# Kernel optimization log

Hardware: AMD Instinct MI355X
Metric: run time of the kernel (lower is better)

The kernel has to match this reference:

```python
import jax, jax.numpy as jnp
import numpy as np

DN = ('NCHW', 'OIHW', 'NCHW')

def _conv(x, w, stride, pad, groups=1):
    return jax.lax.conv_general_dilated(x, w, (stride, stride), pad,
                                        feature_group_count=groups,
                                        dimension_numbers=DN)

def _bn(x, s, b):
    # eval-mode BatchNorm folded to per-channel affine
    return x * s[:, None, None] + b[:, None, None]

def _gelu(x):
    return jax.nn.gelu(x, approximate=False)  # torch nn.GELU default = exact erf

def _region_dw(x, dw_w, s1, b1, pw_w, s2, b2, g):
    # Vectorized RegionLayerDW: split [B,C,H,W] into g*g tiles, apply per-tile
    # depthwise3x3 -> BN -> GELU -> 1x1 -> BN -> +residual, reassemble.
    B, C, H, W = x.shape
    th, tw = H // g, W // g
    t = x.reshape(B, C, g, th, g, tw).transpose(2, 4, 0, 1, 3, 5)
    t = t.reshape(g * g, B, C, th, tw)  # [G,B,C,th,tw]
    def tile(xt, w, ts1, tb1, pw, ts2, tb2):
        h = _conv(xt, w, 1, ((1, 1), (1, 1)), groups=C)  # depthwise 3x3
        h = _gelu(_bn(h, ts1, tb1))
        h = jnp.einsum('bchw,oc->bohw', h, pw)  # 1x1 conv
        return _bn(h, ts2, tb2) + xt
    y = jax.vmap(tile)(t, dw_w, s1, b1, pw_w, s2, b2)
    y = y.reshape(g, g, B, C, th, tw).transpose(2, 3, 0, 4, 1, 5)
    return y.reshape(B, C, H, W)

def _forward(x, r1_w, r1_s, r1_b, r1_dw, r1_s1, r1_b1, r1_pw, r1_s2, r1_b2,
             r2_w, r2_s, r2_b, r2_dw, r2_s1, r2_b1, r2_pw, r2_s2, r2_b2,
             h1_w1, h1_s1, h1_b1, h1_w2, h1_s2, h1_b2, h1_w3, h1_s3, h1_b3,
             h2_w1, h2_s1, h2_b1, h2_w2, h2_s2, h2_b2,
             h3_w, h3_s, h3_b):
    B = x.shape[0]
    # region1: 5x5 conv 3->24, BN, GELU, RegionLayerDW grid 7x7; then outer GELU
    r1 = _gelu(_bn(_conv(x, r1_w, 1, ((2, 2), (2, 2))), r1_s, r1_b))
    r1 = _region_dw(r1, r1_dw, r1_s1, r1_b1, r1_pw, r1_s2, r1_b2, 7)
    region1 = _gelu(r1)
    # region2: 3x3 conv 24->48, BN, GELU, RegionLayerDW grid 4x4; outer GELU
    r2 = _gelu(_bn(_conv(region1, r2_w, 1, ((1, 1), (1, 1))), r2_s, r2_b))
    r2 = _region_dw(r2, r2_dw, r2_s1, r2_b1, r2_pw, r2_s2, r2_b2, 4)
    region2 = _gelu(r2)
    # hMLP branch1: 3 -> 48(k4s4) -> 48(k2s2) -> 256(k2s2)
    h = _gelu(_bn(_conv(x, h1_w1, 4, 'VALID'), h1_s1, h1_b1))
    h = _gelu(_bn(_conv(h, h1_w2, 2, 'VALID'), h1_s2, h1_b2))
    branch1 = _bn(_conv(h, h1_w3, 2, 'VALID'), h1_s3, h1_b3)
    # hMLP branch2: 24 -> 48(k4s4) -> 256(k4s4)
    g2 = _gelu(_bn(_conv(region1, h2_w1, 4, 'VALID'), h2_s1, h2_b1))
    branch2 = _bn(_conv(g2, h2_w2, 4, 'VALID'), h2_s2, h2_b2)
    # hMLP branch3: 48 -> 256(k16s16)
    branch3 = _bn(_conv(region2, h3_w, 16, 'VALID'), h3_s, h3_b)
    out = jnp.concatenate((branch1, branch2, branch3), axis=1)  # [B,768,14,14]
    return jnp.transpose(out.reshape(B, out.shape[1], -1), (0, 2, 1))  # [B,196,768]


def setup_inputs() -> dict:
    key = jax.random.key(0)
    ks = [key]
    def nk():
        ks[0], k = jax.random.split(ks[0])
        return k
    def rn(shape, scale=0.05):
        return jax.random.normal(nk(), shape, jnp.float32) * scale
    def sc(shape):
        return 1.0 + rn(shape)
    B = 16
    d = {}
    d['x'] = rn((B, 3, 224, 224), 1.0)
    d['r1_w'] = rn((24, 3, 5, 5)); d['r1_s'] = sc((24,)); d['r1_b'] = rn((24,))
    d['r1_dw'] = rn((49, 24, 1, 3, 3)); d['r1_s1'] = sc((49, 24)); d['r1_b1'] = rn((49, 24))
    d['r1_pw'] = rn((49, 24, 24)); d['r1_s2'] = sc((49, 24)); d['r1_b2'] = rn((49, 24))
    d['r2_w'] = rn((48, 24, 3, 3)); d['r2_s'] = sc((48,)); d['r2_b'] = rn((48,))
    d['r2_dw'] = rn((16, 48, 1, 3, 3)); d['r2_s1'] = sc((16, 48)); d['r2_b1'] = rn((16, 48))
    d['r2_pw'] = rn((16, 48, 48)); d['r2_s2'] = sc((16, 48)); d['r2_b2'] = rn((16, 48))
    d['h1_w1'] = rn((48, 3, 4, 4)); d['h1_s1'] = sc((48,)); d['h1_b1'] = rn((48,))
    d['h1_w2'] = rn((48, 48, 2, 2)); d['h1_s2'] = sc((48,)); d['h1_b2'] = rn((48,))
    d['h1_w3'] = rn((256, 48, 2, 2)); d['h1_s3'] = sc((256,)); d['h1_b3'] = rn((256,))
    d['h2_w1'] = rn((48, 24, 4, 4)); d['h2_s1'] = sc((48,)); d['h2_b1'] = rn((48,))
    d['h2_w2'] = rn((256, 48, 4, 4)); d['h2_s2'] = sc((256,)); d['h2_b2'] = rn((256,))
    d['h3_w'] = rn((256, 48, 16, 16)); d['h3_s'] = sc((256,)); d['h3_b'] = rn((256,))
    return d


def reference(x, r1_w, r1_s, r1_b, r1_dw, r1_s1, r1_b1, r1_pw, r1_s2, r1_b2,
              r2_w, r2_s, r2_b, r2_dw, r2_s1, r2_b1, r2_pw, r2_s2, r2_b2,
              h1_w1, h1_s1, h1_b1, h1_w2, h1_s2, h1_b2, h1_w3, h1_s3, h1_b3,
              h2_w1, h2_s1, h2_b1, h2_w2, h2_s2, h2_b2,
              h3_w, h3_s, h3_b):
    return _forward(x, r1_w, r1_s, r1_b, r1_dw, r1_s1, r1_b1, r1_pw, r1_s2, r1_b2,
                    r2_w, r2_s, r2_b, r2_dw, r2_s1, r2_b1, r2_pw, r2_s2, r2_b2,
                    h1_w1, h1_s1, h1_b1, h1_w2, h1_s2, h1_b2, h1_w3, h1_s3, h1_b3,
                    h2_w1, h2_s1, h2_b1, h2_w2, h2_s2, h2_b2,
                    h3_w, h3_s, h3_b)
```

## Files before the change

kernel.cpp:

```cpp
#include <hip/hip_runtime.h>
#include <hip/hip_bf16.h>
#include <math.h>

typedef __attribute__((ext_vector_type(8))) short short8;
typedef __attribute__((ext_vector_type(4))) float f32x4;

__device__ __forceinline__ float gelu_f(float x) {
  float s = x * x;
  float w = __builtin_fmaf(s, 0.10294196f, 2.30220795f);
  float e = __builtin_amdgcn_exp2f(x * w);
  float r = __builtin_amdgcn_rcpf(1.0f + e);
  return __builtin_fmaf(-x, r, x);
}

template<bool TBL, bool GELU, bool TOOUT>
__global__ __launch_bounds__(256) void convgemm_k(
    const float* __restrict__ in, const float* __restrict__ w,
    const float* __restrict__ bns, const float* __restrict__ bnb,
    float* __restrict__ out,
    int Cin, int H, int W, int ks, int stride, int pad, int ls,
    int OH, int OW, int N, int K, int ch0) {
  __shared__ __align__(16) float sA[16][64];
  __shared__ __align__(16) float sB[16][64];
  __shared__ int sTbl[256];
  const int tid = threadIdx.x;
  if (TBL) {
    int kk2 = ks * ks;
    for (int k = tid; k < K; k += 256) {
      int ic = k / kk2, r = k - ic * kk2;
      sTbl[k] = (ic << 16) | ((r / ks) << 8) | (r % ks);
    }
  }
  const int m0 = blockIdx.x * 64, n0 = blockIdx.y * 64;
  const int mm = tid >> 2, kq = tid & 3;
  const int OHW = OH * OW, HW = H * W;
  int m = m0 + mm;
  int bI = m / OHW; int r = m - bI * OHW;
  int oh = r / OW;  int ow = r - oh * OW;
  const int ihBase = oh * stride - pad, iwBase = ow * stride - pad;
  const int inBase = bI * Cin * HW;
  const int tm = tid & 15, tn = tid >> 4;
  float acc[4][4] = {};
  for (int k0 = 0; k0 < K; k0 += 16) {
    __syncthreads();
#pragma unroll
    for (int i = 0; i < 4; ++i) {
      int kk = kq * 4 + i, k = k0 + kk;
      float v = 0.0f;
      if (k < K) {
        int ic, dy, dx;
        if (TBL) {
          int tv = sTbl[k]; ic = tv >> 16; dy = (tv >> 8) & 255; dx = tv & 255;
        } else {
          ic = k >> (2 * ls);
          int r2 = k & ((1 << (2 * ls)) - 1);
          dy = r2 >> ls; dx = r2 & ((1 << ls) - 1);
        }
        int ih = ihBase + dy, iw = iwBase + dx;
        if (ih >= 0 && ih < H && iw >= 0 && iw < W)
          v = in[inBase + ic * HW + ih * W + iw];
      }
      sA[kk][mm] = v;
    }
#pragma unroll
    for (int i = 0; i < 4; ++i) {
      int kk = kq * 4 + i, k = k0 + kk;
      int n = n0 + mm;
      float v = 0.0f;
      if (n < N && k < K) v = w[n * K + k];
      sB[kk][mm] = v;
    }
    __syncthreads();
#pragma unroll
    for (int kk = 0; kk < 16; ++kk) {
      float4 a4 = *(const float4*)&sA[kk][tm * 4];
      float4 b4 = *(const float4*)&sB[kk][tn * 4];
      acc[0][0] += a4.x * b4.x; acc[0][1] += a4.x * b4.y;
      acc[0][2] += a4.x * b4.z; acc[0][3] += a4.x * b4.w;
      acc[1][0] += a4.y * b4.x; acc[1][1] += a4.y * b4.y;
      acc[1][2] += a4.y * b4.z; acc[1][3] += a4.y * b4.w;
      acc[2][0] += a4.z * b4.x; acc[2][1] += a4.z * b4.y;
      acc[2][2] += a4.z * b4.z; acc[2][3] += a4.z * b4.w;
      acc[3][0] += a4.w * b4.x; acc[3][1] += a4.w * b4.y;
      acc[3][2] += a4.w * b4.z; acc[3][3] += a4.w * b4.w;
    }
  }
#pragma unroll
  for (int i = 0; i < 4; ++i) {
    int mI = m0 + tm * 4 + i;
    int bO = mI / OHW; int rr = mI - bO * OHW;
#pragma unroll
    for (int j = 0; j < 4; ++j) {
      int n = n0 + tn * 4 + j;
      if (n < N) {
        float v = acc[i][j] * bns[n] + bnb[n];
        if (GELU) v = gelu_f(v);
        if (TOOUT) {
          out[(bO * OHW + rr) * 768 + ch0 + n] = v;
        } else {
          int oh2 = rr / OW, ow2 = rr - oh2 * OW;
          out[((bO * N + n) * OH + oh2) * OW + ow2] = v;
        }
      }
    }
  }
}

template<int CIN, int KS, int STRIDE, int PAD, int NN, int KP, bool GELU,
         int OUTMODE, int NVALID = NN>
__global__ __launch_bounds__(256) void nhwc_conv_mfma(
    const __hip_bfloat16* __restrict__ in, const __hip_bfloat16* __restrict__ wb,
    const float* __restrict__ bns, const float* __restrict__ bnb,
    float* __restrict__ out, int Hin, int Win, int OW, int OHW) {
  constexpr int K = KS * KS * CIN;
  constexpr int LROW = KP + 8;
  __shared__ __align__(16) __hip_bfloat16 sA[64][LROW];
  __shared__ __align__(16) __hip_bfloat16 sB[NN][LROW];
  const int tid = threadIdx.x;
  const float4 f4z = make_float4(0.f, 0.f, 0.f, 0.f);
  if constexpr (CIN == 4) {
    const int m = tid & 63, tg = tid >> 6;
    const int mg = blockIdx.x * 64 + m;
    const int bI = mg / OHW; int pix = mg - bI * OHW;
    const int oh = pix / OW, ow = pix - oh * OW;
    for (int dy = tg; dy < KS; dy += 4) {
      const int ih = oh * STRIDE - PAD + dy;
      __hip_bfloat16* dst = &sA[m][dy * KS * 4];
#pragma unroll
      for (int j = 0; j < KS; ++j) {
        int iw = ow * STRIDE - PAD + j;
        uint2 v = make_uint2(0u, 0u);
        if (ih >= 0 && ih < Hin && iw >= 0 && iw < Win)
          v = *(const uint2*)(in + (((size_t)bI * Hin + ih) * Win + iw) * 4);
        *(uint2*)(dst + j * 4) = v;
      }
    }
    if (tg == 3) {
      for (int c = K; c < KP; c += 4) *(uint2*)&sA[m][c] = make_uint2(0u, 0u);
    }
  } else {
    const int m = tid & 63, dy = tid >> 6;
    const int mg = blockIdx.x * 64 + m;
    const int bI = mg / OHW; int pix = mg - bI * OHW;
    const int oh = pix / OW, ow = pix - oh * OW;
    if (dy < KS) {
      const int ih = oh * STRIDE - PAD + dy;
      __hip_bfloat16* dst = &sA[m][dy * KS * CIN];
      if (ih < 0 || ih >= Hin) {
#pragma unroll
        for (int i = 0; i < KS * CIN / 8; ++i) ((float4*)dst)[i] = f4z;
      } else {
        const __hip_bfloat16* srow = in + ((size_t)bI * Hin + ih) * Win * CIN;
#pragma unroll
        for (int j = 0; j < KS; ++j) {
          int iw = ow * STRIDE - PAD + j;
          if (PAD > 0 && (iw < 0 || iw >= Win)) {
#pragma unroll
            for (int i = 0; i < CIN / 8; ++i) ((float4*)(dst + j * CIN))[i] = f4z;
          } else {
            const float4* s4 = (const float4*)(srow + (size_t)iw * CIN);
#pragma unroll
            for (int i = 0; i < CIN / 8; ++i) ((float4*)(dst + j * CIN))[i] = s4[i];
          }
        }
      }
    } else if (K < KP) {
#pragma unroll
      for (int c = K; c < KP + 8; c += 8) *(float4*)&sA[m][c] = f4z;
    }
  }
  {
    constexpr int NV = NN * KP / 8;
    const float4* w4 = (const float4*)wb;
    for (int i = tid; i < NV; i += 256) {
      int n = i / (KP / 8), c = i - n * (KP / 8);
      *(float4*)&sB[n][c * 8] = w4[i];
    }
  }
  __syncthreads();
  constexpr int NT = NN / 16;
  const int wave = tid >> 6, lane = tid & 63;
  const int fm = lane & 15, quad = lane >> 4;
  const int wm = wave * 16;
  f32x4 acc[NT] = {};
#pragma unroll
  for (int ks = 0; ks < KP / 32; ++ks) {
    short8 a = *(const short8*)&sA[wm + fm][ks * 32 + quad * 8];
#pragma unroll
    for (int j = 0; j < NT; ++j) {
      short8 b = *(const short8*)&sB[j * 16 + fm][ks * 32 + quad * 8];
      acc[j] = __builtin_amdgcn_mfma_f32_16x16x32_bf16(a, b, acc[j], 0, 0, 0);
    }
  }
  const int mg0 = blockIdx.x * 64 + wm + quad * 4;
  const int bI = mg0 / OHW, pix = mg0 - bI * OHW;
#pragma unroll
  for (int j = 0; j < NT; ++j) {
    int n = j * 16 + fm;
    if (n >= NVALID) continue;
    float s = bns[n], bb = bnb[n];
    float v[4];
#pragma unroll
    for (int e = 0; e < 4; ++e) {
      v[e] = acc[j][e] * s + bb;
      if (GELU) v[e] = gelu_f(v[e]);
    }
    if (OUTMODE == 0) {
      float4 v4 = make_float4(v[0], v[1], v[2], v[3]);
      *(float4*)&out[((size_t)(bI * NVALID + n)) * OHW + pix] = v4;
    } else {
      __hip_bfloat16* ob = (__hip_bfloat16*)out;
#pragma unroll
      for (int e = 0; e < 4; ++e)
        ob[((size_t)(bI * OHW + pix + e)) * NVALID + n] = (__hip_bfloat16)v[e];
    }
  }
}

__global__ __launch_bounds__(256, 4) void conv5_tile_mfma(
    const __hip_bfloat16* __restrict__ in,
    const __hip_bfloat16* __restrict__ wb,
    const float* __restrict__ bns, const float* __restrict__ bnb,
    __hip_bfloat16* __restrict__ out) {
  __shared__ __align__(16) __hip_bfloat16 sHalo[13][144];
  __shared__ __align__(16) __hip_bfloat16 sW5[32][128];
  __shared__ float sS[24], sBb[24];
  const int tid = threadIdx.x;
  const int X0 = blockIdx.x * 32, Y0 = blockIdx.y * 8, b = blockIdx.z;
  {
    const float4* w4 = (const float4*)wb;
    for (int i = tid; i < 512; i += 256) {
      int n = i >> 4, g = i & 15;
      *(float4*)&sW5[n][(g ^ (n & 7)) * 8] = w4[i];
    }
  }
  if (tid < 24) { sS[tid] = bns[tid]; sBb[tid] = bnb[tid]; }
  for (int i = tid; i < 468; i += 256) {
    int r = i / 36, p = i - r * 36;
    int iy = Y0 - 2 + r, ix = X0 - 2 + p;
    uint2 v = make_uint2(0u, 0u);
    if (r < 12 && iy >= 0 && iy < 224 && ix >= 0 && ix < 224)
      v = *(const uint2*)(in + (((size_t)b * 224 + iy) * 224 + ix) * 4);
    *(uint2*)&sHalo[r][p * 4] = v;
  }
  __syncthreads();
  const int wave = tid >> 6, lane = tid & 63;
  const int fm = lane & 15, quad = lane >> 4;
  f32x4 acc[4][2] = {};
#pragma unroll
  for (int ks = 0; ks < 4; ++ks) {
    const int k0 = ks * 32 + quad * 8;
    const int dy = k0 / 24, u = k0 - dy * 24;
    const int grp = ks * 4 + quad;
    short8 wfr[2];
#pragma unroll
    for (int cg = 0; cg < 2; ++cg) {
      int wr = cg * 16 + fm;
      wfr[cg] = *(const short8*)&sW5[wr][(grp ^ (wr & 7)) * 8];
    }
#pragma unroll
    for (int pg = 0; pg < 4; ++pg) {
      const int r = 2 * wave + (pg >> 1);
      const int c = (pg & 1) * 16 + fm;
      short8 pf = *(const short8*)&sHalo[r + dy][c * 4 + u];
#pragma unroll
      for (int cg = 0; cg < 2; ++cg)
        acc[pg][cg] = __builtin_amdgcn_mfma_f32_16x16x32_bf16(
            wfr[cg], pf, acc[pg][cg], 0, 0, 0);
    }
  }
#pragma unroll
  for (int pg = 0; pg < 4; ++pg) {
    const int row = Y0 + 2 * wave + (pg >> 1);
    const int col = X0 + (pg & 1) * 16 + fm;
    __hip_bfloat16* obase = out + (((size_t)b * 224 + row) * 224 + col) * 24;
#pragma unroll
    for (int cg = 0; cg < 2; ++cg) {
      const int ch0 = cg * 16 + quad * 4;
      if (ch0 < 24) {
        __hip_bfloat16 vb[4];
#pragma unroll
        for (int e = 0; e < 4; ++e) {
          float v = acc[pg][cg][e] * sS[ch0 + e] + sBb[ch0 + e];
          vb[e] = (__hip_bfloat16)gelu_f(v);
        }
        *(uint2*)&obase[ch0] = *(uint2*)vb;
      }
    }
  }
}

__global__ __launch_bounds__(256, 4) void conv3_tile_mfma(
    const __hip_bfloat16* __restrict__ in,
    const __hip_bfloat16* __restrict__ wb,
    const float* __restrict__ bns, const float* __restrict__ bnb,
    __hip_bfloat16* __restrict__ out) {
  __shared__ __align__(16) __hip_bfloat16 sIn[11][816];
  __shared__ __align__(16) __hip_bfloat16 sB[48][232];
  __shared__ float sS[48], sBb[48];
  const int tid = threadIdx.x;
  const int X0 = blockIdx.x * 32, Y0 = blockIdx.y * 8, b = blockIdx.z;
  {
    const float4* w4 = (const float4*)wb;
    for (int i = tid; i < 1344; i += 256) {
      int n = i / 28, c = i - n * 28;
      *(float4*)&sB[n][c * 8] = w4[i];
    }
  }
  if (tid < 48) { sS[tid] = bns[tid]; sBb[tid] = bnb[tid]; }
  for (int i = tid; i < 1020; i += 256) {
    int r = i / 102, c8 = i - r * 102;
    int p = c8 / 3;
    int iy = Y0 - 1 + r, ix = X0 - 1 + p;
    uint4 v = make_uint4(0u, 0u, 0u, 0u);
    if (iy >= 0 && iy < 224 && ix >= 0 && ix < 224)
      v = *(const uint4*)(in + (((size_t)b * 224 + iy) * 224 + ix) * 24 +
                          (c8 - p * 3) * 8);
    *(uint4*)&sIn[r][c8 * 8] = v;
  }
  for (int i = tid; i < 102; i += 256)
    *(uint4*)&sIn[10][i * 8] = make_uint4(0u, 0u, 0u, 0u);
  __syncthreads();
  const int wave = tid >> 6, lane = tid & 63;
  const int fm = lane & 15, quad = lane >> 4;
  f32x4 acc[4][3] = {};
#pragma unroll
  for (int ks = 0; ks < 7; ++ks) {
    const int k0 = ks * 32 + quad * 8;
    const int dy = k0 / 72;
    const int u = k0 - dy * 72;
    short8 wfr[3];
#pragma unroll
    for (int cg = 0; cg < 3; ++cg)
      wfr[cg] = *(const short8*)&sB[cg * 16 + fm][k0];
#pragma unroll
    for (int pg = 0; pg < 4; ++pg) {
      const int r = 2 * wave + (pg >> 1);
      const int c = (pg & 1) * 16 + fm;
      short8 pf = *(const short8*)&sIn[r + dy][c * 24 + u];
#pragma unroll
      for (int cg = 0; cg < 3; ++cg)
        acc[pg][cg] = __builtin_amdgcn_mfma_f32_16x16x32_bf16(
            wfr[cg], pf, acc[pg][cg], 0, 0, 0);
    }
  }
#pragma unroll
  for (int pg = 0; pg < 4; ++pg) {
    const int row = Y0 + 2 * wave + (pg >> 1);
    const int col = X0 + (pg & 1) * 16 + fm;
    __hip_bfloat16* obase = out + (((size_t)b * 224 + row) * 224 + col) * 48;
#pragma unroll
    for (int cg = 0; cg < 3; ++cg) {
      const int ch0 = cg * 16 + quad * 4;
      __hip_bfloat16 vb[4];
#pragma unroll
      for (int e = 0; e < 4; ++e) {
        const int ch = ch0 + e;
        float v = acc[pg][cg][e] * sS[ch] + sBb[ch];
        vb[e] = (__hip_bfloat16)gelu_f(v);
      }
      *(uint2*)&obase[ch0] = *(uint2*)vb;
    }
  }
}

__global__ __launch_bounds__(256, 4) void region2_mfma(
    const __hip_bfloat16* __restrict__ in, const float* __restrict__ dww,
    const float* __restrict__ s1v, const float* __restrict__ b1v,
    const __hip_bfloat16* __restrict__ pwb,
    const float* __restrict__ s2v, const float* __restrict__ b2v,
    __hip_bfloat16* __restrict__ out) {
  __shared__ __align__(16) __hip_bfloat16 sIn[10][10][56];
  __shared__ __align__(16) __hip_bfloat16 sH[64][64];
  __shared__ __align__(16) __hip_bfloat16 sW[48][64];
  __shared__ float sDW[48][9];
  __shared__ float sS1[48], sB1[48], sS2[48], sB2[48];
  const int t = blockIdx.x, sb = blockIdx.y, b = blockIdx.z;
  const int gy = t >> 2, gx = t & 3;
  const int py0 = (sb / 7) * 8, px0 = (sb % 7) * 8;
  const int Y0 = gy * 56, X0 = gx * 56;
  const int tid = threadIdx.x;
  for (int i = tid; i < 48 * 8; i += 256) {
    int n = i >> 3, g = i & 7;
    float4 v = *(const float4*)&pwb[(size_t)(t * 48 + n) * 64 + g * 8];
    *(float4*)&sW[n][((g ^ (n & 7)) * 8)] = v;
  }
  for (int i = tid; i < 432; i += 256) ((float*)sDW)[i] = dww[t * 432 + i];
  if (tid < 48) {
    sS1[tid] = s1v[t * 48 + tid]; sB1[tid] = b1v[t * 48 + tid];
    sS2[tid] = s2v[t * 48 + tid]; sB2[tid] = b2v[t * 48 + tid];
  }
  for (int i = tid; i < 600; i += 256) {
    int px = i / 6, grp = i - px * 6;
    int r = px / 10, c = px - r * 10;
    int ly = py0 + r - 1, lx = px0 + c - 1;
    uint4 v = make_uint4(0u, 0u, 0u, 0u);
    if (ly >= 0 && ly < 56 && lx >= 0 && lx < 56)
      v = *(const uint4*)(in + (((size_t)b * 224 + Y0 + ly) * 224 + X0 + lx) * 48 +
                          grp * 8);
    *(uint4*)&sIn[r][c][grp * 8] = v;
  }
  __syncthreads();
  if (tid < 192) {
    const int cg = tid >> 4;
    const int rem = tid & 15;
    const int col = rem >> 1;
    const int rh = rem & 1;
    const int ch0 = cg * 4;
    float wv[4][9], s14[4], b14[4];
#pragma unroll
    for (int c4 = 0; c4 < 4; ++c4) {
#pragma unroll
      for (int q = 0; q < 9; ++q) wv[c4][q] = sDW[ch0 + c4][q];
      s14[c4] = sS1[ch0 + c4]; b14[c4] = sB1[ch0 + c4];
    }
    float win[3][12];
#pragma unroll
    for (int rr = 0; rr < 6; ++rr) {
      int r = rh * 4 + rr;
      float* wr = win[rr % 3];
#pragma unroll
      for (int cc = 0; cc < 3; ++cc) {
        uint2 u = *(const uint2*)&sIn[r][col + cc][ch0];
        wr[cc * 4 + 0] = __uint_as_float(u.x << 16);
        wr[cc * 4 + 1] = __uint_as_float(u.x & 0xffff0000u);
        wr[cc * 4 + 2] = __uint_as_float(u.y << 16);
        wr[cc * 4 + 3] = __uint_as_float(u.y & 0xffff0000u);
      }
      if (rr >= 2) {
        const float* ra = win[(rr - 2) % 3];
        const float* rb = win[(rr - 1) % 3];
        const float* rc = win[rr % 3];
        int px = (rh * 4 + rr - 2) * 8 + col;
        __hip_bfloat16 hv[4];
#pragma unroll
        for (int c4 = 0; c4 < 4; ++c4) {
          float a = ra[c4] * wv[c4][0] + ra[4 + c4] * wv[c4][1] + ra[8 + c4] * wv[c4][2]
                  + rb[c4] * wv[c4][3] + rb[4 + c4] * wv[c4][4] + rb[8 + c4] * wv[c4][5]
                  + rc[c4] * wv[c4][6] + rc[4 + c4] * wv[c4][7] + rc[8 + c4] * wv[c4][8];
          hv[c4] = (__hip_bfloat16)gelu_f(a * s14[c4] + b14[c4]);
        }
        *(uint2*)&sH[px][((cg >> 1) ^ (px & 7)) * 8 + (cg & 1) * 4] = *(uint2*)hv;
      }
    }
  } else {
    for (int i = tid - 192; i < 128; i += 64) {
      int px = i >> 1, g = 6 + (i & 1);
      *(float4*)&sH[px][(g ^ (px & 7)) * 8] = make_float4(0.f, 0.f, 0.f, 0.f);
    }
  }
  __syncthreads();
  const int wave = tid >> 6, lane = tid & 63;
  const int fm = lane & 15, quad = lane >> 4;
  const int px = wave * 16 + fm, pxk = px & 7;
  f32x4 acc[3] = {};
#pragma unroll
  for (int ks = 0; ks < 2; ++ks) {
    short8 hb = *(const short8*)&sH[px][((ks * 4 + quad) ^ pxk) * 8];
#pragma unroll
    for (int m = 0; m < 3; ++m) {
      int wr = m * 16 + fm;
      short8 wa = *(const short8*)&sW[wr][((ks * 4 + quad) ^ (wr & 7)) * 8];
      acc[m] = __builtin_amdgcn_mfma_f32_16x16x32_bf16(wa, hb, acc[m], 0, 0, 0);
    }
  }
  const int row = px >> 3, col = px & 7;
  __hip_bfloat16* obase =
      out + (((size_t)b * 224 + Y0 + py0 + row) * 224 + X0 + px0 + col) * 48;
#pragma unroll
  for (int m = 0; m < 3; ++m) {
    int ch0m = m * 16 + quad * 4;
    uint2 ru = *(const uint2*)&sIn[row + 1][col + 1][ch0m];
    float res[4];
    res[0] = __uint_as_float(ru.x << 16);
    res[1] = __uint_as_float(ru.x & 0xffff0000u);
    res[2] = __uint_as_float(ru.y << 16);
    res[3] = __uint_as_float(ru.y & 0xffff0000u);
    __hip_bfloat16 vb[4];
#pragma unroll
    for (int e = 0; e < 4; ++e) {
      int ch = ch0m + e;
      float v = acc[m][e] * sS2[ch] + sB2[ch] + res[e];
      vb[e] = (__hip_bfloat16)gelu_f(v);
    }
    *(uint2*)&obase[ch0m] = *(uint2*)vb;
  }
}

__global__ __launch_bounds__(256, 4) void region1_mfma(
    const __hip_bfloat16* __restrict__ in, const float* __restrict__ dww,
    const float* __restrict__ s1v, const float* __restrict__ b1v,
    const __hip_bfloat16* __restrict__ pwb,
    const float* __restrict__ s2v, const float* __restrict__ b2v,
    __hip_bfloat16* __restrict__ out) {
  __shared__ __align__(16) __hip_bfloat16 sIn[10][10][24];
  __shared__ __align__(16) __hip_bfloat16 sH[64][32];
  __shared__ __align__(16) __hip_bfloat16 sW[32][32];
  __shared__ float sDW[24][9];
  __shared__ float sS1[24], sB1[24], sS2[24], sB2[24];
  const int t = blockIdx.x, sb = blockIdx.y, b = blockIdx.z;
  const int gy = t / 7, gx = t % 7;
  const int py0 = (sb >> 2) * 8, px0 = (sb & 3) * 8;
  const int Y0 = gy * 32, X0 = gx * 32;
  const int tid = threadIdx.x;
  for (int i = tid; i < 128; i += 256) {
    int n = i >> 2, g = i & 3;
    float4 v = make_float4(0.f, 0.f, 0.f, 0.f);
    if (n < 24) v = *(const float4*)&pwb[(size_t)(t * 24 + n) * 32 + g * 8];
    *(float4*)&sW[n][(g ^ (n & 3)) * 8] = v;
  }
  for (int i = tid; i < 216; i += 256) ((float*)sDW)[i] = dww[t * 216 + i];
  if (tid < 24) {
    sS1[tid] = s1v[t * 24 + tid]; sB1[tid] = b1v[t * 24 + tid];
    sS2[tid] = s2v[t * 24 + tid]; sB2[tid] = b2v[t * 24 + tid];
  }
  for (int i = tid; i < 300; i += 256) {
    int px = i / 3, grp = i - px * 3;
    int r = px / 10, c = px - r * 10;
    int ly = py0 + r - 1, lx = px0 + c - 1;
    uint4 v = make_uint4(0u, 0u, 0u, 0u);
    if (ly >= 0 && ly < 32 && lx >= 0 && lx < 32)
      v = *(const uint4*)(in + (((size_t)b * 224 + Y0 + ly) * 224 + X0 + lx) * 24 +
                          grp * 8);
    *(uint4*)&sIn[r][c][grp * 8] = v;
  }
  __syncthreads();
  if (tid < 192) {
    const int cg = tid >> 5;
    const int rem = tid & 31;
    const int col = rem >> 2;
    const int rq = rem & 3;
    const int ch0 = cg * 4;
    float wv[4][9], s14[4], b14[4];
#pragma unroll
    for (int c4 = 0; c4 < 4; ++c4) {
#pragma unroll
      for (int q = 0; q < 9; ++q) wv[c4][q] = sDW[ch0 + c4][q];
      s14[c4] = sS1[ch0 + c4]; b14[c4] = sB1[ch0 + c4];
    }
    float win[3][12];
#pragma unroll
    for (int rr = 0; rr < 4; ++rr) {
      int r = rq * 2 + rr;
      float* wr = win[rr % 3];
#pragma unroll
      for (int cc = 0; cc < 3; ++cc) {
        uint2 u = *(const uint2*)&sIn[r][col + cc][ch0];
        wr[cc * 4 + 0] = __uint_as_float(u.x << 16);
        wr[cc * 4 + 1] = __uint_as_float(u.x & 0xffff0000u);
        wr[cc * 4 + 2] = __uint_as_float(u.y << 16);
        wr[cc * 4 + 3] = __uint_as_float(u.y & 0xffff0000u);
      }
      if (rr >= 2) {
        const float* ra = win[(rr - 2) % 3];
        const float* rb = win[(rr - 1) % 3];
        const float* rc = win[rr % 3];
        int px = (rq * 2 + rr - 2) * 8 + col;
        __hip_bfloat16 hv[4];
#pragma unroll
        for (int c4 = 0; c4 < 4; ++c4) {
          float a = ra[c4] * wv[c4][0] + ra[4 + c4] * wv[c4][1] + ra[8 + c4] * wv[c4][2]
                  + rb[c4] * wv[c4][3] + rb[4 + c4] * wv[c4][4] + rb[8 + c4] * wv[c4][5]
                  + rc[c4] * wv[c4][6] + rc[4 + c4] * wv[c4][7] + rc[8 + c4] * wv[c4][8];
          hv[c4] = (__hip_bfloat16)gelu_f(a * s14[c4] + b14[c4]);
        }
        *(uint2*)&sH[px][((cg >> 1) ^ (px & 3)) * 8 + (cg & 1) * 4] = *(uint2*)hv;
      }
    }
  } else {
    int px = tid - 192;
    *(float4*)&sH[px][(3 ^ (px & 3)) * 8] = make_float4(0.f, 0.f, 0.f, 0.f);
  }
  __syncthreads();
  const int wave = tid >> 6, lane = tid & 63;
  const int fm = lane & 15, quad = lane >> 4;
  const int px = wave * 16 + fm;
  short8 hb = *(const short8*)&sH[px][(quad ^ (px & 3)) * 8];
  f32x4 acc[2] = {};
#pragma unroll
  for (int m = 0; m < 2; ++m) {
    int wr = m * 16 + fm;
    short8 wa = *(const short8*)&sW[wr][(quad ^ (wr & 3)) * 8];
    acc[m] = __builtin_amdgcn_mfma_f32_16x16x32_bf16(wa, hb, acc[m], 0, 0, 0);
  }
  const int row = px >> 3, col = px & 7;
  __hip_bfloat16* obase =
      out + (((size_t)b * 224 + Y0 + py0 + row) * 224 + X0 + px0 + col) * 24;
#pragma unroll
  for (int m = 0; m < 2; ++m) {
    int ch0m = m * 16 + quad * 4;
    if (ch0m < 24) {
      uint2 ru = *(const uint2*)&sIn[row + 1][col + 1][ch0m];
      float res[4];
      res[0] = __uint_as_float(ru.x << 16);
      res[1] = __uint_as_float(ru.x & 0xffff0000u);
      res[2] = __uint_as_float(ru.y << 16);
      res[3] = __uint_as_float(ru.y & 0xffff0000u);
      __hip_bfloat16 vb[4];
#pragma unroll
      for (int e = 0; e < 4; ++e) {
        int ch = ch0m + e;
        float v = acc[m][e] * sS2[ch] + sB2[ch] + res[e];
        vb[e] = (__hip_bfloat16)gelu_f(v);
      }
      *(uint2*)&obase[ch0m] = *(uint2*)vb;
    }
  }
}

template<int PS, int IMGW, int KTOT, int KSL, bool ATOMIC>
__global__ __launch_bounds__(256) void patch_gemm_mfma(
    const __hip_bfloat16* __restrict__ A, const __hip_bfloat16* __restrict__ Wb,
    const float* __restrict__ scale, const float* __restrict__ bias,
    float* __restrict__ out, int M, int ch0) {
  constexpr int RUN = PS * 48;
  __shared__ __align__(16) __hip_bfloat16 sA[64][64];
  __shared__ __align__(16) __hip_bfloat16 sB[64][64];
  const int tid = threadIdx.x;
  const int m0 = blockIdx.x * 64, n0 = blockIdx.y * 64;
  const int kBase = blockIdx.z * KSL;
  const int mi = tid >> 2, seg = tid & 3;
  int m = m0 + mi; int mc = (m < M) ? m : (M - 1);
  int bI = mc / 196; int r = mc - bI * 196;
  int oh = r / 14, ow = r - oh * 14;
  const __hip_bfloat16* Abase =
      A + (((size_t)bI * IMGW + oh * PS) * IMGW + ow * PS) * 48;
  const __hip_bfloat16* Wrow = Wb + (size_t)(n0 + mi) * KTOT;
  const int wave = tid >> 6, lane = tid & 63;
  const int wm = (wave & 1) * 32, wn = (wave >> 1) * 32;
  const int fm = lane & 15, quad = lane >> 4;
  const int sw = fm & 7;
  f32x4 acc[2][2] = {};
  for (int k0 = kBase; k0 < kBase + KSL; k0 += 64) {
    int dy = k0 / RUN, rem = k0 - dy * RUN;
    __syncthreads();
    {
      const __hip_bfloat16* p = Abase + (size_t)dy * IMGW * 48 + rem + seg * 16;
      float4 v0 = *(const float4*)p;
      float4 v1 = *(const float4*)(p + 8);
      int key = mi & 7;
      *(float4*)&sA[mi][((seg * 2) ^ key) * 8] = v0;
      *(float4*)&sA[mi][((seg * 2 + 1) ^ key) * 8] = v1;
      const __hip_bfloat16* q = Wrow + k0 + seg * 16;
      float4 w0 = *(const float4*)q;
      float4 w1 = *(const float4*)(q + 8);
      *(float4*)&sB[mi][((seg * 2) ^ key) * 8] = w0;
      *(float4*)&sB[mi][((seg * 2 + 1) ^ key) * 8] = w1;
    }
    __syncthreads();
#pragma unroll
    for (int ks = 0; ks < 2; ++ks) {
      int cg = (ks * 4 + quad) ^ sw;
#pragma unroll
      for (int i = 0; i < 2; ++i) {
        short8 a = *(const short8*)&sA[wm + i * 16 + fm][cg * 8];
#pragma unroll
        for (int j = 0; j < 2; ++j) {
          short8 b = *(const short8*)&sB[wn + j * 16 + fm][cg * 8];
          acc[i][j] = __builtin_amdgcn_mfma_f32_16x16x32_bf16(a, b, acc[i][j], 0, 0, 0);
        }
      }
    }
  }
#pragma unroll
  for (int i = 0; i < 2; ++i) {
#pragma unroll
    for (int j = 0; j < 2; ++j) {
      int gn = n0 + wn + j * 16 + fm;
      float sc = scale[gn];
#pragma unroll
      for (int e = 0; e < 4; ++e) {
        int gm = m0 + wm + i * 16 + quad * 4 + e;
        if (gm < M) {
          if (ATOMIC)
            atomicAdd(&out[(size_t)gm * 768 + ch0 + gn], acc[i][j][e] * sc);
          else
            out[(size_t)gm * 768 + ch0 + gn] = acc[i][j][e] * sc + bias[gn];
        }
      }
    }
  }
}

__device__ __forceinline__ void reorder_wk_el(
    const float* __restrict__ w, __hip_bfloat16* __restrict__ o,
    int i, int N, int Cin, int ks, int KP) {
  if (i >= N * KP) return;
  int n = i / KP, k = i - n * KP;
  float v = 0.f;
  int K = ks * ks * Cin;
  if (k < K) {
    int dy = k / (ks * Cin); int r = k - dy * ks * Cin;
    int dx = r / Cin, ic = r - dx * Cin;
    v = w[((n * Cin + ic) * ks + dy) * ks + dx];
  }
  o[i] = (__hip_bfloat16)v;
}

__global__ __launch_bounds__(256) void prep_all(
    const float* __restrict__ x, __hip_bfloat16* __restrict__ xb,
    const float* __restrict__ h3_w, __hip_bfloat16* __restrict__ h3wb,
    const float* __restrict__ r2_w, __hip_bfloat16* __restrict__ r2wb,
    const float* __restrict__ h2_w1, __hip_bfloat16* __restrict__ h2w1b,
    const float* __restrict__ h2_w2, __hip_bfloat16* __restrict__ h2w2b,
    const float* __restrict__ r1_w, __hip_bfloat16* __restrict__ r1wb,
    const float* __restrict__ r2_pw, __hip_bfloat16* __restrict__ pw2wb,
    const float* __restrict__ r1_pw, __hip_bfloat16* __restrict__ pw1wb,
    const float* __restrict__ h1_w1, __hip_bfloat16* __restrict__ h1w1b,
    const float* __restrict__ h3_b, float* __restrict__ out) {
  __shared__ __hip_bfloat16 sL[12288];
  const int blk = blockIdx.x, tid = threadIdx.x;
  if (blk < 3136) {
    int i = blk * 256 + tid;
    int b = i / 50176, p = i - b * 50176;
    const float* src = x + (size_t)b * 150528 + p;
    __hip_bfloat16 v[4];
    v[0] = (__hip_bfloat16)src[0];
    v[1] = (__hip_bfloat16)src[50176];
    v[2] = (__hip_bfloat16)src[100352];
    v[3] = (__hip_bfloat16)0.0f;
    *(uint2*)&xb[(size_t)i * 4] = *(uint2*)v;
  } else if (blk < 3392) {
    int n = blk - 3136;
    const float* src = h3_w + (size_t)n * 12288;
    for (int j = tid; j < 12288; j += 256) sL[j] = (__hip_bfloat16)src[j];
    __syncthreads();
    __hip_bfloat16* dst = h3wb + (size_t)n * 12288;
    for (int k = tid; k < 12288; k += 256) {
      int dy = k / 768, rem = k - dy * 768;
      int dx = rem / 48, ic = rem - dx * 48;
      dst[k] = sL[ic * 256 + dy * 16 + dx];
    }
  } else if (blk < 3434) {
    reorder_wk_el(r2_w, r2wb, (blk - 3392) * 256 + tid, 48, 24, 3, 224);
  } else if (blk < 3506) {
    reorder_wk_el(h2_w1, h2w1b, (blk - 3434) * 256 + tid, 48, 24, 4, 384);
  } else if (blk < 4274) {
    reorder_wk_el(h2_w2, h2w2b, (blk - 3506) * 256 + tid, 256, 48, 4, 768);
  } else if (blk < 4290) {
    int i = (blk - 4274) * 256 + tid;
    int n = i >> 7, k = i & 127;
    int dy = k / 24, u = k - dy * 24;
    float v = 0.f;
    if (n < 24 && dy < 5 && u < 20) {
      int dx = u >> 2, ic = u & 3;
      if (ic < 3) v = r1_w[((n * 3 + ic) * 5 + dy) * 5 + dx];
    }
    r1wb[i] = (__hip_bfloat16)v;
  } else if (blk < 4482) {
    int i = (blk - 4290) * 256 + tid;
    int t = i / 3072, r = i - t * 3072;
    int n = r >> 6, k = r & 63;
    float v = (k < 48) ? r2_pw[(t * 48 + n) * 48 + k] : 0.f;
    pw2wb[i] = (__hip_bfloat16)v;
  } else if (blk < 4629) {
    int i = (blk - 4482) * 256 + tid;
    int t = i / 768, r = i - t * 768;
    int n = r >> 5, k = r & 31;
    float v = (k < 24) ? r1_pw[(t * 24 + n) * 24 + k] : 0.f;
    pw1wb[i] = (__hip_bfloat16)v;
  } else if (blk < 4641) {
    int i = (blk - 4629) * 256 + tid;
    int n = i >> 6, k = i & 63;
    int dy = k >> 4, r = k & 15;
    int dx = r >> 2, ic = r & 3;
    float v = 0.f;
    if (ic < 3) v = h1_w1[((n * 3 + ic) * 4 + dy) * 4 + dx];
    h1w1b[i] = (__hip_bfloat16)v;
  } else {
    int i = (blk - 4641) * 256 + tid;
    int n = i & 255, bp = i >> 8;
    out[bp * 768 + 512 + n] = h3_b[n];
  }
}

extern "C" void kernel_launch(void* const* d_in, const int* in_sizes, int n_in,
                              void* d_out, int out_size, void* d_ws, size_t ws_size,
                              hipStream_t stream) {
  const float* x     = (const float*)d_in[0];
  const float* r1_w  = (const float*)d_in[1];
  const float* r1_s  = (const float*)d_in[2];
  const float* r1_b  = (const float*)d_in[3];
  const float* r1_dw = (const float*)d_in[4];
  const float* r1_s1 = (const float*)d_in[5];
  const float* r1_b1 = (const float*)d_in[6];
  const float* r1_pw = (const float*)d_in[7];
  const float* r1_s2 = (const float*)d_in[8];
  const float* r1_b2 = (const float*)d_in[9];
  const float* r2_w  = (const float*)d_in[10];
  const float* r2_s  = (const float*)d_in[11];
  const float* r2_b  = (const float*)d_in[12];
  const float* r2_dw = (const float*)d_in[13];
  const float* r2_s1 = (const float*)d_in[14];
  const float* r2_b1 = (const float*)d_in[15];
  const float* r2_pw = (const float*)d_in[16];
  const float* r2_s2 = (const float*)d_in[17];
  const float* r2_b2 = (const float*)d_in[18];
  const float* h1_w1 = (const float*)d_in[19];
  const float* h1_s1 = (const float*)d_in[20];
  const float* h1_b1 = (const float*)d_in[21];
  const float* h1_w2 = (const float*)d_in[22];
  const float* h1_s2 = (const float*)d_in[23];
  const float* h1_b2 = (const float*)d_in[24];
  const float* h1_w3 = (const float*)d_in[25];
  const float* h1_s3 = (const float*)d_in[26];
  const float* h1_b3 = (const float*)d_in[27];
  const float* h2_w1 = (const float*)d_in[28];
  const float* h2_s1 = (const float*)d_in[29];
  const float* h2_b1 = (const float*)d_in[30];
  const float* h2_w2 = (const float*)d_in[31];
  const float* h2_s2 = (const float*)d_in[32];
  const float* h2_b2 = (const float*)d_in[33];
  const float* h3_w  = (const float*)d_in[34];
  const float* h3_s  = (const float*)d_in[35];
  const float* h3_b  = (const float*)d_in[36];
  float* out = (float*)d_out;

  float* F = (float*)d_ws;
  __hip_bfloat16* R1b   = (__hip_bfloat16*)F;
  __hip_bfloat16* C5b   = (__hip_bfloat16*)(F + 9633792);
  __hip_bfloat16* T1b   = (__hip_bfloat16*)(F + 9633792);
  __hip_bfloat16* T2b   = (__hip_bfloat16*)(F + 28901376);
  __hip_bfloat16* h3wb  = (__hip_bfloat16*)(F + 48168960);
  __hip_bfloat16* r2wb  = (__hip_bfloat16*)(F + 49741824);
  __hip_bfloat16* h2w1b = (__hip_bfloat16*)(F + 49747200);
  __hip_bfloat16* pw2wb = (__hip_bfloat16*)(F + 49756416);
  __hip_bfloat16* r1wb  = (__hip_bfloat16*)(F + 49780992);
  __hip_bfloat16* h2w2b = (__hip_bfloat16*)(F + 49783040);
  __hip_bfloat16* xb    = (__hip_bfloat16*)(F + 49881344);
  __hip_bfloat16* S1b   = (__hip_bfloat16*)(F + 51486976);
  float* S1             = F + 52691200;
  float* S2             = F + 55099648;
  __hip_bfloat16* pw1wb = (__hip_bfloat16*)(F + 55701760);
  __hip_bfloat16* h1w1b = (__hip_bfloat16*)(F + 55720576);

  dim3 blk(256);

  prep_all<<<dim3(7777), blk, 0, stream>>>(
      x, xb, h3_w, h3wb, r2_w, r2wb, h2_w1, h2w1b, h2_w2, h2w2b,
      r1_w, r1wb, r2_pw, pw2wb, r1_pw, pw1wb, h1_w1, h1w1b, h3_b, out);

  conv5_tile_mfma<<<dim3(7, 28, 16), blk, 0, stream>>>(
      xb, r1wb, r1_s, r1_b, C5b);
  region1_mfma<<<dim3(49, 16, 16), blk, 0, stream>>>(
      C5b, r1_dw, r1_s1, r1_b1, pw1wb, r1_s2, r1_b2, R1b);
  nhwc_conv_mfma<24, 4, 4, 0, 48, 384, true, 1><<<dim3(784), blk, 0, stream>>>(
      R1b, h2w1b, h2_s1, h2_b1, (float*)S1b, 224, 224, 56, 3136);
  patch_gemm_mfma<4, 56, 768, 768, false><<<dim3(49, 4, 1), blk, 0, stream>>>(
      S1b, h2w2b, h2_s2, h2_b2, out, 3136, 256);
  nhwc_conv_mfma<4, 4, 4, 0, 48, 64, true, 0><<<dim3(784), blk, 0, stream>>>(
      xb, h1w1b, h1_s1, h1_b1, S1, 224, 224, 56, 3136);
  convgemm_k<false, true, false><<<dim3(196, 1), blk, 0, stream>>>(
      S1, h1_w2, h1_s2, h1_b2, S2, 48, 56, 56, 2, 2, 0, 1, 28, 28, 48, 192, 0);
  convgemm_k<false, false, true><<<dim3(49, 4), blk, 0, stream>>>(
      S2, h1_w3, h1_s3, h1_b3, out, 48, 28, 28, 2, 2, 0, 1, 14, 14, 256, 192, 0);
  conv3_tile_mfma<<<dim3(7, 28, 16), blk, 0, stream>>>(
      R1b, r2wb, r2_s, r2_b, T1b);
  region2_mfma<<<dim3(16, 49, 16), blk, 0, stream>>>(
      T1b, r2_dw, r2_s1, r2_b1, pw2wb, r2_s2, r2_b2, T2b);
  patch_gemm_mfma<16, 224, 12288, 1536, true><<<dim3(49, 4, 8), blk, 0, stream>>>(
      T2b, h3wb, h3_s, h3_b, out, 3136, 512);
  (void)in_sizes; (void)n_in; (void)out_size; (void)ws_size;
}
```

Measured before the change: 495.8 us.

## Add full-N 64x256 MFMA patch GEMM for branch3 and pad weight-transpose LDS

```diff
diff --git a/kernel.cpp b/kernel.cpp
--- a/kernel.cpp
+++ b/kernel.cpp
@@ -682,6 +682,77 @@
   }
 }
 
+__global__ __launch_bounds__(256) void patch_gemm_b3(
+    const __hip_bfloat16* __restrict__ A,
+    const __hip_bfloat16* __restrict__ Wb,
+    const float* __restrict__ scale, float* __restrict__ out) {
+  __shared__ __align__(16) __hip_bfloat16 sA[64][64];
+  __shared__ __align__(16) __hip_bfloat16 sB[256][64];
+  const int tid = threadIdx.x;
+  const int m0 = blockIdx.x * 64;
+  const int kBase = blockIdx.y * 1536;
+  const int mi = tid >> 2, seg = tid & 3;
+  int m = m0 + mi;
+  int bI = m / 196; int r = m - bI * 196;
+  int oh = r / 14, ow = r - oh * 14;
+  const __hip_bfloat16* Abase =
+      A + (((size_t)bI * 224 + oh * 16) * 224 + ow * 16) * 48;
+  const __hip_bfloat16* Wrow = Wb + (size_t)tid * 12288;
+  const int wave = tid >> 6, lane = tid & 63;
+  const int wn = wave * 64;
+  const int fm = lane & 15, quad = lane >> 4;
+  const int sw = fm & 7;
+  const int wkey = tid & 7;
+  f32x4 acc[4][4] = {};
+  for (int k0 = kBase; k0 < kBase + 1536; k0 += 64) {
+    int dy = k0 / 768, rem = k0 - dy * 768;
+    __syncthreads();
+    {
+      const __hip_bfloat16* p = Abase + (size_t)dy * 224 * 48 + rem + seg * 16;
+      float4 v0 = *(const float4*)p;
+      float4 v1 = *(const float4*)(p + 8);
+      int key = mi & 7;
+      *(float4*)&sA[mi][((seg * 2) ^ key) * 8] = v0;
+      *(float4*)&sA[mi][((seg * 2 + 1) ^ key) * 8] = v1;
+      const __hip_bfloat16* q = Wrow + k0;
+#pragma unroll
+      for (int j = 0; j < 8; ++j) {
+        float4 wv = *(const float4*)(q + j * 8);
+        *(float4*)&sB[tid][(j ^ wkey) * 8] = wv;
+      }
+    }
+    __syncthreads();
+#pragma unroll
+    for (int ks = 0; ks < 2; ++ks) {
+      int cg = (ks * 4 + quad) ^ sw;
+      short8 a[4];
+#pragma unroll
+      for (int i = 0; i < 4; ++i)
+        a[i] = *(const short8*)&sA[i * 16 + fm][cg * 8];
+#pragma unroll
+      for (int j = 0; j < 4; ++j) {
+        short8 b = *(const short8*)&sB[wn + j * 16 + fm][cg * 8];
+#pragma unroll
+        for (int i = 0; i < 4; ++i)
+          acc[i][j] = __builtin_amdgcn_mfma_f32_16x16x32_bf16(a[i], b, acc[i][j], 0, 0, 0);
+      }
+    }
+  }
+#pragma unroll
+  for (int i = 0; i < 4; ++i) {
+#pragma unroll
+    for (int j = 0; j < 4; ++j) {
+      int gn = wn + j * 16 + fm;
+      float sc = scale[gn];
+#pragma unroll
+      for (int e = 0; e < 4; ++e) {
+        int gm = m0 + i * 16 + quad * 4 + e;
+        atomicAdd(&out[(size_t)gm * 768 + 512 + gn], acc[i][j][e] * sc);
+      }
+    }
+  }
+}
+
 __device__ __forceinline__ void reorder_wk_el(
     const float* __restrict__ w, __hip_bfloat16* __restrict__ o,
     int i, int N, int Cin, int ks, int KP) {
@@ -708,7 +779,7 @@
     const float* __restrict__ r1_pw, __hip_bfloat16* __restrict__ pw1wb,
     const float* __restrict__ h1_w1, __hip_bfloat16* __restrict__ h1w1b,
     const float* __restrict__ h3_b, float* __restrict__ out) {
-  __shared__ __hip_bfloat16 sL[12288];
+  __shared__ __hip_bfloat16 sL[48 * 258];
   const int blk = blockIdx.x, tid = threadIdx.x;
   if (blk < 3136) {
     int i = blk * 256 + tid;
@@ -723,13 +794,14 @@
   } else if (blk < 3392) {
     int n = blk - 3136;
     const float* src = h3_w + (size_t)n * 12288;
-    for (int j = tid; j < 12288; j += 256) sL[j] = (__hip_bfloat16)src[j];
+    for (int j = tid; j < 12288; j += 256)
+      sL[(j >> 8) * 258 + (j & 255)] = (__hip_bfloat16)src[j];
     __syncthreads();
     __hip_bfloat16* dst = h3wb + (size_t)n * 12288;
     for (int k = tid; k < 12288; k += 256) {
       int dy = k / 768, rem = k - dy * 768;
       int dx = rem / 48, ic = rem - dx * 48;
-      dst[k] = sL[ic * 256 + dy * 16 + dx];
+      dst[k] = sL[ic * 258 + dy * 16 + dx];
     }
   } else if (blk < 3434) {
     reorder_wk_el(r2_w, r2wb, (blk - 3392) * 256 + tid, 48, 24, 3, 224);
@@ -858,7 +930,7 @@
       R1b, r2wb, r2_s, r2_b, T1b);
   region2_mfma<<<dim3(16, 49, 16), blk, 0, stream>>>(
       T1b, r2_dw, r2_s1, r2_b1, pw2wb, r2_s2, r2_b2, T2b);
-  patch_gemm_mfma<16, 224, 12288, 1536, true><<<dim3(49, 4, 8), blk, 0, stream>>>(
-      T2b, h3wb, h3_s, h3_b, out, 3136, 512);
+  patch_gemm_b3<<<dim3(49, 8), blk, 0, stream>>>(
+      T2b, h3wb, h3_s, out);
   (void)in_sizes; (void)n_in; (void)out_size; (void)ws_size;
 }
```

New measurement: 468.1 us (median of 2 runs). -5.6%, faster.
